# Optimization experiments

Hardware: AMD Instinct MI355X
Metric: run time of the kernel (lower is better)

The kernel has to match this reference:

```python
import jax, jax.numpy as jnp
import numpy as np
from jax import lax

IN, H1, H2, F1, OUT = 26, 64, 32, 16, 10
B, T = 512, 1000


def _lstm(x, w_ih, w_hh, b_ih, b_hh):
    """PyTorch-convention LSTM (gate order i,f,g,o). x: [B,T,I].
    Returns (all hidden states [B,T,H], final hidden [B,H])."""
    Bx = x.shape[0]
    H = w_hh.shape[1]
    # Precompute input projections for all timesteps: [B,T,4H]
    xg = jnp.einsum('bti,gi->btg', x, w_ih) + b_ih + b_hh

    def step(carry, xg_t):
        h, c = carry
        gates = xg_t + h @ w_hh.T  # [B,4H]
        i, f, g, o = jnp.split(gates, 4, axis=-1)
        i = jax.nn.sigmoid(i)
        f = jax.nn.sigmoid(f)
        g = jnp.tanh(g)
        o = jax.nn.sigmoid(o)
        c = f * c + i * g
        h = o * jnp.tanh(c)
        return (h, c), h

    init = (jnp.zeros((Bx, H), x.dtype), jnp.zeros((Bx, H), x.dtype))
    (h_last, _), hs = lax.scan(step, init, xg.transpose(1, 0, 2))
    return hs.transpose(1, 0, 2), h_last


def setup_inputs() -> dict:
    key = jax.random.key(0)
    ks = jax.random.split(key, 14)

    def u(k, shape, fan):
        bound = 1.0 / np.sqrt(fan)
        return jax.random.uniform(k, shape, jnp.float32, -bound, bound)

    return {
        'x': jax.random.normal(ks[0], (B, 1, IN, T), jnp.float32),
        'w_ih1': u(ks[1], (4 * H1, IN), H1),
        'w_hh1': u(ks[2], (4 * H1, H1), H1),
        'b_ih1': u(ks[3], (4 * H1,), H1),
        'b_hh1': u(ks[4], (4 * H1,), H1),
        'w_ih2': u(ks[5], (4 * H2, H1), H2),
        'w_hh2': u(ks[6], (4 * H2, H2), H2),
        'b_ih2': u(ks[7], (4 * H2,), H2),
        'b_hh2': u(ks[8], (4 * H2,), H2),
        'w_fc1': u(ks[9], (F1, H2), H2),
        'b_fc1': u(ks[10], (F1,), H2),
        'w_fc2': u(ks[11], (OUT, F1), F1),
        'b_fc2': u(ks[12], (OUT,), F1),
    }


def reference(x, w_ih1, w_hh1, b_ih1, b_hh1, w_ih2, w_hh2, b_ih2, b_hh2,
              w_fc1, b_fc1, w_fc2, b_fc2):
    # [B,1,26,T] -> [B,26,T] -> [B,T,26]
    x = jnp.transpose(x[:, 0], (0, 2, 1))
    out1, _ = _lstm(x, w_ih1, w_hh1, b_ih1, b_hh1)
    # Dropout is identity in eval mode.
    _, h2 = _lstm(out1, w_ih2, w_hh2, b_ih2, b_hh2)  # final hidden [B,32]
    h = jax.nn.relu(h2 @ w_fc1.T + b_fc1)
    return h @ w_fc2.T + b_fc2  # [B,10]
```

## Files before the change

kernel.cpp:

```cpp
#include <hip/hip_runtime.h>
#include <hip/hip_bf16.h>


typedef __hip_bfloat16 bf16;
typedef _Float16 f16;
typedef _Float16 f16x8 __attribute__((ext_vector_type(8)));
typedef _Float16 f16x4 __attribute__((ext_vector_type(4)));
typedef float    f32x4 __attribute__((ext_vector_type(4)));

#define T_STEPS 1000
#define IN_DIM  26
#define EPB     16
#define CH      16
#define NCHUNK  62
#define H1P     72
#define H2P     40
#define XP      40

#define NL2E  -1.4426950408889634f
#define N2L2E -2.8853900817779268f

__device__ __forceinline__ float bits2f(unsigned short h) {
    return __uint_as_float(((unsigned int)h) << 16);
}
__device__ __forceinline__ float ldv(const void* p, long i, bool isb) {
    return isb ? bits2f(((const unsigned short*)p)[i]) : ((const float*)p)[i];
}
__device__ __forceinline__ float rcp_(float x) { return __builtin_amdgcn_rcpf(x); }
__device__ __forceinline__ float ex2_(float x) { return __builtin_amdgcn_exp2f(x); }

__device__ __forceinline__ float lstm_act(float yi, float yf, float yg,
                                          float yo, float& c) {
    const float A  = ex2_(yi), F = ex2_(yf), B = ex2_(yg), O = ex2_(yo);
    const float a1 = 1.f + A, f1 = 1.f + F, b1 = 1.f + B, o1 = 1.f + O;
    const float ig = (2.f - b1) * rcp_(a1 * b1);
    c = fmaf(rcp_(f1), c, ig);
    const float C2  = ex2_(N2L2E * c);
    const float c1p = 1.f + C2;
    return (2.f - c1p) * rcp_(o1 * c1p);
}

#define MFMA(a, b, c) __builtin_amdgcn_mfma_f32_16x16x32_f16((a), (b), (c), 0, 0, 0)

__global__
__attribute__((amdgpu_flat_work_group_size(512, 512), amdgpu_waves_per_eu(2, 2)))
void lstm_fused(const void* __restrict__ x,
                const void* __restrict__ w_ih1, const void* __restrict__ w_hh1,
                const void* __restrict__ b_ih1, const void* __restrict__ b_hh1,
                const void* __restrict__ w_ih2, const void* __restrict__ w_hh2,
                const void* __restrict__ b_ih2, const void* __restrict__ b_hh2,
                const void* __restrict__ w_fc1, const void* __restrict__ b_fc1,
                const void* __restrict__ w_fc2, const void* __restrict__ b_fc2,
                void* __restrict__ out)
{
    const int tid  = threadIdx.x;
    const int lane = tid & 63;
    const int wv   = tid >> 6;
    const int ecol = lane & 15;
    const int g4   = lane >> 4;
    const int r15  = lane & 15;
    const int e0   = blockIdx.x * EPB;

    __shared__ __align__(16) f16   Xst[2][CH][EPB][XP];
    __shared__ __align__(16) f16   H1T[2][EPB][H1P];
    __shared__ __align__(16) f16   H2T[2][EPB][H2P];
    __shared__ __align__(16) float f1s[EPB][16];

    bool isb = true;
    {
        const unsigned short* wu = (const unsigned short*)w_ih1;
        for (int k = 0; k < 64; ++k) {
            float v = fabsf(bits2f(wu[k]));
            if (!(v <= 0.1251f)) isb = false;
        }
    }

    {
        float4 z; z.x = z.y = z.z = z.w = 0.f;
        float4* p = (float4*)&Xst[0][0][0][0];
        for (int k = tid; k < (int)(sizeof(Xst) / 16); k += 512) p[k] = z;
        float4* q = (float4*)&H1T[0][0][0];
        for (int k = tid; k < (int)(sizeof(H1T) / 16); k += 512) q[k] = z;
        float4* r = (float4*)&H2T[0][0][0];
        for (int k = tid; k < (int)(sizeof(H2T) / 16); k += 512) r[k] = z;
    }

    f16x8 W8[8]; f16x8 W4[4]; f32x4 C4[4];
    if (wv < 4) {
#pragma unroll
        for (int gi = 0; gi < 4; ++gi) {
            const float sc = (gi == 2) ? N2L2E : NL2E;
            const int R = gi * 64 + 16 * wv + r15;
#pragma unroll
            for (int k0 = 0; k0 < 2; ++k0)
#pragma unroll
                for (int jj = 0; jj < 8; ++jj)
                    W8[gi * 2 + k0][jj] =
                        (f16)(sc * ldv(w_hh1, R * 64 + k0 * 32 + g4 * 8 + jj, isb));
#pragma unroll
            for (int jj = 0; jj < 8; ++jj) {
                const int k = g4 * 8 + jj;
                W4[gi][jj] =
                    (f16)(k < IN_DIM ? sc * ldv(w_ih1, R * IN_DIM + k, isb) : 0.f);
            }
#pragma unroll
            for (int jj = 0; jj < 4; ++jj) {
                const int Rc = gi * 64 + 16 * wv + g4 * 4 + jj;
                C4[gi][jj] = sc * (ldv(b_ih1, Rc, isb) + ldv(b_hh1, Rc, isb));
            }
        }
    } else if (wv < 6) {
        const int hf = wv - 4;
#pragma unroll
        for (int gi = 0; gi < 4; ++gi) {
            const float sc = (gi == 2) ? N2L2E : NL2E;
            const int R = gi * 32 + 16 * hf + r15;
#pragma unroll
            for (int k0 = 0; k0 < 2; ++k0)
#pragma unroll
                for (int jj = 0; jj < 8; ++jj)
                    W8[gi * 2 + k0][jj] =
                        (f16)(sc * ldv(w_ih2, R * 64 + k0 * 32 + g4 * 8 + jj, isb));
#pragma unroll
            for (int jj = 0; jj < 8; ++jj)
                W4[gi][jj] = (f16)(sc * ldv(w_hh2, R * 32 + g4 * 8 + jj, isb));
#pragma unroll
            for (int jj = 0; jj < 4; ++jj) {
                const int Rc = gi * 32 + 16 * hf + g4 * 4 + jj;
                C4[gi][jj] = sc * (ldv(b_ih2, Rc, isb) + ldv(b_hh2, Rc, isb));
            }
        }
    }

    __syncthreads();

    auto stageRow = [&](int p, int c) {
        const int t0 = c * CH;
        const int nt = (T_STEPS - t0 < CH) ? (T_STEPS - t0) : CH;
        const int e = p / IN_DIM, i = p - e * IN_DIM;
        const long gb = ((long)(e0 + e) * IN_DIM + i) * T_STEPS + t0;
        float4 fb[4];
        if (isb) {
            const float4* q = (const float4*)((const unsigned short*)x + gb);
            fb[0] = q[0]; if (nt > 8) fb[1] = q[1];
        } else {
            const float4* q = (const float4*)((const float*)x + gb);
            fb[0] = q[0]; fb[1] = q[1];
            if (nt > 8) { fb[2] = q[2]; fb[3] = q[3]; }
        }
#pragma unroll
        for (int t = 0; t < CH; ++t) if (t < nt) {
            float v;
            if (isb) {
                unsigned int u =
                    __builtin_bit_cast(unsigned int, fb[t >> 3][(t >> 1) & 3]);
                v = bits2f((t & 1) ? (unsigned short)(u >> 16)
                                   : (unsigned short)(u & 0xffffu));
            } else {
                v = fb[t >> 2][t & 3];
            }
            Xst[c & 1][t][e][i] = (f16)v;
        }
    };

    if (tid < EPB * IN_DIM) stageRow(tid, 0);
    if (tid >= 448 && tid < 448 + 26) stageRow(tid - 448, 1);
    __syncthreads();

    f32x4 xgc[4];
    if (wv < 4) {
        const f16x8 xf = *(const f16x8*)&Xst[0][0][ecol][g4 * 8];
#pragma unroll
        for (int gi = 0; gi < 4; ++gi) xgc[gi] = MFMA(W4[gi], xf, C4[gi]);
    }

    if (wv < 6) __builtin_amdgcn_s_setprio(1);

    float cst[4] = {0.f, 0.f, 0.f, 0.f};

    for (int s = 0; s <= T_STEPS; ++s) {
        const int pc = s & 1, pp = pc ^ 1;

        if (wv < 4) {
            if (s < T_STEPS) {
                const f16x8 h1f0 = *(const f16x8*)&H1T[pp][ecol][g4 * 8];
                const f16x8 h1f1 = *(const f16x8*)&H1T[pp][ecol][32 + g4 * 8];
                const bool nx = (s + 1 < T_STEPS);
                f16x8 xf = {};
                if (nx) {
                    const int sn = s + 1;
                    xf = *(const f16x8*)&Xst[(sn >> 4) & 1][sn & 15][ecol][g4 * 8];
                }
                f32x4 gt[4];
#pragma unroll
                for (int gi = 0; gi < 4; ++gi) {
                    f32x4 t0 = MFMA(W8[gi * 2 + 0], h1f0, xgc[gi]);
                    gt[gi]   = MFMA(W8[gi * 2 + 1], h1f1, t0);
                }
                f32x4 xgn[4];
                if (nx) {
#pragma unroll
                    for (int gi = 0; gi < 4; ++gi)
                        xgn[gi] = MFMA(W4[gi], xf, C4[gi]);
                }
                f16x4 hh;
#pragma unroll
                for (int jj = 0; jj < 4; ++jj)
                    hh[jj] = (f16)lstm_act(gt[0][jj], gt[1][jj],
                                           gt[2][jj], gt[3][jj], cst[jj]);
                *(f16x4*)&H1T[pc][ecol][16 * wv + g4 * 4] = hh;
                if (nx) {
#pragma unroll
                    for (int gi = 0; gi < 4; ++gi) xgc[gi] = xgn[gi];
                }
            }
        } else if (wv < 6) {
            if (s >= 1) {
                const int hf = wv - 4;
                const f16x8 h1f0 = *(const f16x8*)&H1T[pp][ecol][g4 * 8];
                const f16x8 h1f1 = *(const f16x8*)&H1T[pp][ecol][32 + g4 * 8];
                const f16x8 h2f  = *(const f16x8*)&H2T[pc][ecol][g4 * 8];
                f32x4 gt[4];
#pragma unroll
                for (int gi = 0; gi < 4; ++gi) {
                    f32x4 t0 = MFMA(W8[gi * 2 + 0], h1f0, C4[gi]);
                    t0       = MFMA(W8[gi * 2 + 1], h1f1, t0);
                    gt[gi]   = MFMA(W4[gi], h2f, t0);
                }
                f16x4 hh;
#pragma unroll
                for (int jj = 0; jj < 4; ++jj)
                    hh[jj] = (f16)lstm_act(gt[0][jj], gt[1][jj],
                                           gt[2][jj], gt[3][jj], cst[jj]);
                *(f16x4*)&H2T[pp][ecol][16 * hf + g4 * 4] = hh;
            }
        } else {
            const int s1 = s + 1, c = (s1 >> 4) + 1;
            if (c <= NCHUNK) {
                const int slice = s1 & 15;
                const int p = slice * 26 + (wv - 6) * 13 + lane;
                if (lane < 13) stageRow(p, c);
            }
        }

        __syncthreads();
    }

    if (tid < EPB * 16) {
        const int e = tid >> 4, o = tid & 15;
        float ss = ldv(b_fc1, o, isb);
#pragma unroll 8
        for (int k = 0; k < 32; ++k)
            ss = fmaf(ldv(w_fc1, o * 32 + k, isb), (float)H2T[1][e][k], ss);
        f1s[e][o] = fmaxf(ss, 0.f);
    }
    __syncthreads();
    if (tid < EPB * 10) {
        const int e = tid / 10, o = tid - e * 10;
        float ss = ldv(b_fc2, o, isb);
#pragma unroll
        for (int k = 0; k < 16; ++k)
            ss = fmaf(ldv(w_fc2, o * 16 + k, isb), f1s[e][k], ss);
        const long oi = (long)(e0 + e) * 10 + o;
        if (isb) ((bf16*)out)[oi] = __float2bfloat16(ss);
        else     ((float*)out)[oi] = ss;
    }
}

extern "C" void kernel_launch(void* const* d_in, const int* in_sizes, int n_in,
                              void* d_out, int out_size, void* d_ws, size_t ws_size,
                              hipStream_t stream) {
    lstm_fused<<<dim3(512 / EPB), dim3(512), 0, stream>>>(
        d_in[0], d_in[1], d_in[2], d_in[3], d_in[4],
        d_in[5], d_in[6], d_in[7], d_in[8],
        d_in[9], d_in[10], d_in[11], d_in[12], d_out);
}
```

Before: 821.7 us.

## Process two 16-sequence groups per block with interleaved layer-1 MFMA chains

Each block now handles 32 sequences as two groups: the four layer-1 waves compute both groups' recurrences interleaved, and waves 4-7 split layer-2 work across the groups instead of waves 6-7 doing input staging. Global staging loads are spread across all waves, issued at loop start and written to LDS after compute to hide latency. The grid halves to 16 blocks, so fewer CUs are used, but the independent X/Y chains give more instruction-level parallelism inside the latency-bound recurrent step. The cost is doubled per-step work for layer-1 waves and higher register pressure.

```diff
diff --git a/kernel.cpp b/kernel.cpp
--- a/kernel.cpp
+++ b/kernel.cpp
@@ -59,12 +59,12 @@
     const int ecol = lane & 15;
     const int g4   = lane >> 4;
     const int r15  = lane & 15;
-    const int e0   = blockIdx.x * EPB;
-
-    __shared__ __align__(16) f16   Xst[2][CH][EPB][XP];
-    __shared__ __align__(16) f16   H1T[2][EPB][H1P];
-    __shared__ __align__(16) f16   H2T[2][EPB][H2P];
-    __shared__ __align__(16) float f1s[EPB][16];
+    const int e00  = blockIdx.x * (2 * EPB);
+
+    __shared__ __align__(16) f16   Xst[2][2][CH][EPB][XP];
+    __shared__ __align__(16) f16   H1T[2][2][EPB][H1P];
+    __shared__ __align__(16) f16   H2T[2][2][EPB][H2P];
+    __shared__ __align__(16) float f1s[2][EPB][16];
 
     bool isb = true;
     {
@@ -77,11 +77,11 @@
 
     {
         float4 z; z.x = z.y = z.z = z.w = 0.f;
-        float4* p = (float4*)&Xst[0][0][0][0];
+        float4* p = (float4*)&Xst[0][0][0][0][0];
         for (int k = tid; k < (int)(sizeof(Xst) / 16); k += 512) p[k] = z;
-        float4* q = (float4*)&H1T[0][0][0];
+        float4* q = (float4*)&H1T[0][0][0][0];
         for (int k = tid; k < (int)(sizeof(H1T) / 16); k += 512) q[k] = z;
-        float4* r = (float4*)&H2T[0][0][0];
+        float4* r = (float4*)&H2T[0][0][0][0];
         for (int k = tid; k < (int)(sizeof(H2T) / 16); k += 512) r[k] = z;
     }
 
@@ -109,8 +109,8 @@
                 C4[gi][jj] = sc * (ldv(b_ih1, Rc, isb) + ldv(b_hh1, Rc, isb));
             }
         }
-    } else if (wv < 6) {
-        const int hf = wv - 4;
+    } else {
+        const int hf = (wv - 4) & 1;
 #pragma unroll
         for (int gi = 0; gi < 4; ++gi) {
             const float sc = (gi == 2) ? N2L2E : NL2E;
@@ -134,11 +134,11 @@
 
     __syncthreads();
 
-    auto stageRow = [&](int p, int c) {
+    auto stageP = [&](int g, int p, int c) {
         const int t0 = c * CH;
         const int nt = (T_STEPS - t0 < CH) ? (T_STEPS - t0) : CH;
         const int e = p / IN_DIM, i = p - e * IN_DIM;
-        const long gb = ((long)(e0 + e) * IN_DIM + i) * T_STEPS + t0;
+        const long gb = ((long)(e00 + g * EPB + e) * IN_DIM + i) * T_STEPS + t0;
         float4 fb[4];
         if (isb) {
             const float4* q = (const float4*)((const unsigned short*)x + gb);
@@ -159,67 +159,107 @@
             } else {
                 v = fb[t >> 2][t & 3];
             }
-            Xst[c & 1][t][e][i] = (f16)v;
+            Xst[g][c & 1][t][e][i] = (f16)v;
         }
     };
 
-    if (tid < EPB * IN_DIM) stageRow(tid, 0);
-    if (tid >= 448 && tid < 448 + 26) stageRow(tid - 448, 1);
+    for (int r = tid; r < 2 * EPB * IN_DIM; r += 512)
+        stageP(r / (EPB * IN_DIM), r % (EPB * IN_DIM), 0);
+    if (tid >= 460) {
+        const int r = tid - 460;
+        stageP(r / IN_DIM, r % IN_DIM, 1);
+    }
     __syncthreads();
 
-    f32x4 xgc[4];
+    f32x4 xgcX[4], xgcY[4];
     if (wv < 4) {
-        const f16x8 xf = *(const f16x8*)&Xst[0][0][ecol][g4 * 8];
-#pragma unroll
-        for (int gi = 0; gi < 4; ++gi) xgc[gi] = MFMA(W4[gi], xf, C4[gi]);
-    }
-
-    if (wv < 6) __builtin_amdgcn_s_setprio(1);
-
+        const f16x8 xfX = *(const f16x8*)&Xst[0][0][0][ecol][g4 * 8];
+        const f16x8 xfY = *(const f16x8*)&Xst[1][0][0][ecol][g4 * 8];
+#pragma unroll
+        for (int gi = 0; gi < 4; ++gi) {
+            xgcX[gi] = MFMA(W4[gi], xfX, C4[gi]);
+            xgcY[gi] = MFMA(W4[gi], xfY, C4[gi]);
+        }
+    }
+
+    float c1X[4] = {0.f, 0.f, 0.f, 0.f};
+    float c1Y[4] = {0.f, 0.f, 0.f, 0.f};
     float cst[4] = {0.f, 0.f, 0.f, 0.f};
+
+    const int srow = wv + 8 * lane;
+    const bool stl = (srow < 52);
+    const int sG = stl ? (srow / IN_DIM) : 0;
+    const int sI = stl ? (srow - sG * IN_DIM) : 0;
 
     for (int s = 0; s <= T_STEPS; ++s) {
         const int pc = s & 1, pp = pc ^ 1;
 
+        const int s1 = s + 1, cS = (s1 >> 4) + 1;
+        const bool doS = stl && (cS <= NCHUNK);
+        float4 fbS[4];
+        int eS = 0, ntS = CH;
+        if (doS) {
+            eS = s1 & 15;
+            const int t0S = cS * CH;
+            ntS = (T_STEPS - t0S < CH) ? (T_STEPS - t0S) : CH;
+            const long gb =
+                ((long)(e00 + sG * EPB + eS) * IN_DIM + sI) * T_STEPS + t0S;
+            if (isb) {
+                const float4* q = (const float4*)((const unsigned short*)x + gb);
+                fbS[0] = q[0]; if (ntS > 8) fbS[1] = q[1];
+            } else {
+                const float4* q = (const float4*)((const float*)x + gb);
+                fbS[0] = q[0]; fbS[1] = q[1];
+                if (ntS > 8) { fbS[2] = q[2]; fbS[3] = q[3]; }
+            }
+        }
+
         if (wv < 4) {
             if (s < T_STEPS) {
-                const f16x8 h1f0 = *(const f16x8*)&H1T[pp][ecol][g4 * 8];
-                const f16x8 h1f1 = *(const f16x8*)&H1T[pp][ecol][32 + g4 * 8];
+                const f16x8 h1f0X = *(const f16x8*)&H1T[0][pp][ecol][g4 * 8];
+                const f16x8 h1f1X = *(const f16x8*)&H1T[0][pp][ecol][32 + g4 * 8];
+                const f16x8 h1f0Y = *(const f16x8*)&H1T[1][pp][ecol][g4 * 8];
+                const f16x8 h1f1Y = *(const f16x8*)&H1T[1][pp][ecol][32 + g4 * 8];
                 const bool nx = (s + 1 < T_STEPS);
-                f16x8 xf = {};
+                f16x8 xfX = {}, xfY = {};
                 if (nx) {
-                    const int sn = s + 1;
-                    xf = *(const f16x8*)&Xst[(sn >> 4) & 1][sn & 15][ecol][g4 * 8];
-                }
-                f32x4 gt[4];
+                    const int sn = s + 1, nb = (sn >> 4) & 1, nt = sn & 15;
+                    xfX = *(const f16x8*)&Xst[0][nb][nt][ecol][g4 * 8];
+                    xfY = *(const f16x8*)&Xst[1][nb][nt][ecol][g4 * 8];
+                }
+                f32x4 gtX[4], gtY[4];
 #pragma unroll
                 for (int gi = 0; gi < 4; ++gi) {
-                    f32x4 t0 = MFMA(W8[gi * 2 + 0], h1f0, xgc[gi]);
-                    gt[gi]   = MFMA(W8[gi * 2 + 1], h1f1, t0);
-                }
-                f32x4 xgn[4];
+                    f32x4 tX = MFMA(W8[gi * 2 + 0], h1f0X, xgcX[gi]);
+                    gtX[gi]  = MFMA(W8[gi * 2 + 1], h1f1X, tX);
+                    f32x4 tY = MFMA(W8[gi * 2 + 0], h1f0Y, xgcY[gi]);
+                    gtY[gi]  = MFMA(W8[gi * 2 + 1], h1f1Y, tY);
+                }
                 if (nx) {
 #pragma unroll
-                    for (int gi = 0; gi < 4; ++gi)
-                        xgn[gi] = MFMA(W4[gi], xf, C4[gi]);
-                }
-                f16x4 hh;
-#pragma unroll
-                for (int jj = 0; jj < 4; ++jj)
-                    hh[jj] = (f16)lstm_act(gt[0][jj], gt[1][jj],
-                                           gt[2][jj], gt[3][jj], cst[jj]);
-                *(f16x4*)&H1T[pc][ecol][16 * wv + g4 * 4] = hh;
-                if (nx) {
-#pragma unroll
-                    for (int gi = 0; gi < 4; ++gi) xgc[gi] = xgn[gi];
-                }
-            }
-        } else if (wv < 6) {
+                    for (int gi = 0; gi < 4; ++gi) {
+                        xgcX[gi] = MFMA(W4[gi], xfX, C4[gi]);
+                        xgcY[gi] = MFMA(W4[gi], xfY, C4[gi]);
+                    }
+                }
+                f16x4 hhX, hhY;
+#pragma unroll
+                for (int jj = 0; jj < 4; ++jj) {
+                    hhX[jj] = (f16)lstm_act(gtX[0][jj], gtX[1][jj],
+                                            gtX[2][jj], gtX[3][jj], c1X[jj]);
+                    hhY[jj] = (f16)lstm_act(gtY[0][jj], gtY[1][jj],
+                                            gtY[2][jj], gtY[3][jj], c1Y[jj]);
+                }
+                *(f16x4*)&H1T[0][pc][ecol][16 * wv + g4 * 4] = hhX;
+                *(f16x4*)&H1T[1][pc][ecol][16 * wv + g4 * 4] = hhY;
+            }
+        } else {
             if (s >= 1) {
-                const int hf = wv - 4;
-                const f16x8 h1f0 = *(const f16x8*)&H1T[pp][ecol][g4 * 8];
-                const f16x8 h1f1 = *(const f16x8*)&H1T[pp][ecol][32 + g4 * 8];
-                const f16x8 h2f  = *(const f16x8*)&H2T[pc][ecol][g4 * 8];
+                const int g  = (wv >= 6) ? 1 : 0;
+                const int hf = (wv - 4) & 1;
+                const f16x8 h1f0 = *(const f16x8*)&H1T[g][pp][ecol][g4 * 8];
+                const f16x8 h1f1 = *(const f16x8*)&H1T[g][pp][ecol][32 + g4 * 8];
+                const f16x8 h2f  = *(const f16x8*)&H2T[g][pc][ecol][g4 * 8];
                 f32x4 gt[4];
 #pragma unroll
                 for (int gi = 0; gi < 4; ++gi) {
@@ -232,36 +272,48 @@
                 for (int jj = 0; jj < 4; ++jj)
                     hh[jj] = (f16)lstm_act(gt[0][jj], gt[1][jj],
                                            gt[2][jj], gt[3][jj], cst[jj]);
-                *(f16x4*)&H2T[pp][ecol][16 * hf + g4 * 4] = hh;
-            }
-        } else {
-            const int s1 = s + 1, c = (s1 >> 4) + 1;
-            if (c <= NCHUNK) {
-                const int slice = s1 & 15;
-                const int p = slice * 26 + (wv - 6) * 13 + lane;
-                if (lane < 13) stageRow(p, c);
+                *(f16x4*)&H2T[g][pp][ecol][16 * hf + g4 * 4] = hh;
+            }
+        }
+
+        if (doS) {
+            const int bf = cS & 1;
+#pragma unroll
+            for (int t = 0; t < CH; ++t) if (t < ntS) {
+                float v;
+                if (isb) {
+                    unsigned int u =
+                        __builtin_bit_cast(unsigned int, fbS[t >> 3][(t >> 1) & 3]);
+                    v = bits2f((t & 1) ? (unsigned short)(u >> 16)
+                                       : (unsigned short)(u & 0xffffu));
+                } else {
+                    v = fbS[t >> 2][t & 3];
+                }
+                Xst[sG][bf][t][eS][sI] = (f16)v;
             }
         }
 
         __syncthreads();
     }
 
-    if (tid < EPB * 16) {
-        const int e = tid >> 4, o = tid & 15;
+    {
+        const int g = tid >> 8, r = tid & 255;
+        const int e = r >> 4, o = r & 15;
         float ss = ldv(b_fc1, o, isb);
 #pragma unroll 8
         for (int k = 0; k < 32; ++k)
-            ss = fmaf(ldv(w_fc1, o * 32 + k, isb), (float)H2T[1][e][k], ss);
-        f1s[e][o] = fmaxf(ss, 0.f);
+            ss = fmaf(ldv(w_fc1, o * 32 + k, isb), (float)H2T[g][1][e][k], ss);
+        f1s[g][e][o] = fmaxf(ss, 0.f);
     }
     __syncthreads();
-    if (tid < EPB * 10) {
-        const int e = tid / 10, o = tid - e * 10;
+    if (tid < 320) {
+        const int g = tid / 160, r = tid - g * 160;
+        const int e = r / 10, o = r - e * 10;
         float ss = ldv(b_fc2, o, isb);
 #pragma unroll
         for (int k = 0; k < 16; ++k)
-            ss = fmaf(ldv(w_fc2, o * 16 + k, isb), f1s[e][k], ss);
-        const long oi = (long)(e0 + e) * 10 + o;
+            ss = fmaf(ldv(w_fc2, o * 16 + k, isb), f1s[g][e][k], ss);
+        const long oi = (long)(e00 + g * EPB + e) * 10 + o;
         if (isb) ((bf16*)out)[oi] = __float2bfloat16(ss);
         else     ((float*)out)[oi] = ss;
     }
@@ -270,7 +322,7 @@
 extern "C" void kernel_launch(void* const* d_in, const int* in_sizes, int n_in,
                               void* d_out, int out_size, void* d_ws, size_t ws_size,
                               hipStream_t stream) {
-    lstm_fused<<<dim3(512 / EPB), dim3(512), 0, stream>>>(
+    lstm_fused<<<dim3(512 / (2 * EPB)), dim3(512), 0, stream>>>(
         d_in[0], d_in[1], d_in[2], d_in[3], d_in[4],
         d_in[5], d_in[6], d_in[7], d_in[8],
         d_in[9], d_in[10], d_in[11], d_in[12], d_out);
```

Result: slower. 2.414 ms (+193.8%).

## Merge LSTM layer roles into four uniform waves, bulk-stage input every chunk

Applied to the files above, without the earlier changes.

Replaces the specialised wave roles (4 layer-1 waves, 2 layer-2 waves, 2 loader waves) with 4 waves that each compute a layer-1 slice and a duplicated layer-2 slice. Each wave applies the activation to half of the layer-2 outputs. Input staging becomes a bulk load of a whole 16-step chunk once every 16 steps. The cell update is rewritten to use one reciprocal instead of two. The aim is fewer waves per barrier and less cost on the serial per-step critical path. The trade-off is redundant layer-2 MFMAs, more registers per wave, and periodic load stalls at chunk boundaries that no longer overlap with compute.

```diff
diff --git a/kernel.cpp b/kernel.cpp
--- a/kernel.cpp
+++ b/kernel.cpp
@@ -6,13 +6,13 @@
 typedef _Float16 f16;
 typedef _Float16 f16x8 __attribute__((ext_vector_type(8)));
 typedef _Float16 f16x4 __attribute__((ext_vector_type(4)));
+typedef _Float16 f16x2 __attribute__((ext_vector_type(2)));
 typedef float    f32x4 __attribute__((ext_vector_type(4)));
 
 #define T_STEPS 1000
 #define IN_DIM  26
 #define EPB     16
 #define CH      16
-#define NCHUNK  62
 #define H1P     72
 #define H2P     40
 #define XP      40
@@ -33,8 +33,9 @@
                                           float yo, float& c) {
     const float A  = ex2_(yi), F = ex2_(yf), B = ex2_(yg), O = ex2_(yo);
     const float a1 = 1.f + A, f1 = 1.f + F, b1 = 1.f + B, o1 = 1.f + O;
-    const float ig = (2.f - b1) * rcp_(a1 * b1);
-    c = fmaf(rcp_(f1), c, ig);
+    const float P  = a1 * b1;
+    const float R  = rcp_(P * f1);
+    c = R * fmaf(c, P, (2.f - b1) * f1);
     const float C2  = ex2_(N2L2E * c);
     const float c1p = 1.f + C2;
     return (2.f - c1p) * rcp_(o1 * c1p);
@@ -43,7 +44,7 @@
 #define MFMA(a, b, c) __builtin_amdgcn_mfma_f32_16x16x32_f16((a), (b), (c), 0, 0, 0)
 
 __global__
-__attribute__((amdgpu_flat_work_group_size(512, 512), amdgpu_waves_per_eu(2, 2)))
+__attribute__((amdgpu_flat_work_group_size(256, 256), amdgpu_waves_per_eu(1, 1)))
 void lstm_fused(const void* __restrict__ x,
                 const void* __restrict__ w_ih1, const void* __restrict__ w_hh1,
                 const void* __restrict__ b_ih1, const void* __restrict__ b_hh1,
@@ -56,6 +57,8 @@
     const int tid  = threadIdx.x;
     const int lane = tid & 63;
     const int wv   = tid >> 6;
+    const int hf   = wv & 1;
+    const int jh   = wv >> 1;
     const int ecol = lane & 15;
     const int g4   = lane >> 4;
     const int r15  = lane & 15;
@@ -78,56 +81,53 @@
     {
         float4 z; z.x = z.y = z.z = z.w = 0.f;
         float4* p = (float4*)&Xst[0][0][0][0];
-        for (int k = tid; k < (int)(sizeof(Xst) / 16); k += 512) p[k] = z;
+        for (int k = tid; k < (int)(sizeof(Xst) / 16); k += 256) p[k] = z;
         float4* q = (float4*)&H1T[0][0][0];
-        for (int k = tid; k < (int)(sizeof(H1T) / 16); k += 512) q[k] = z;
+        for (int k = tid; k < (int)(sizeof(H1T) / 16); k += 256) q[k] = z;
         float4* r = (float4*)&H2T[0][0][0];
-        for (int k = tid; k < (int)(sizeof(H2T) / 16); k += 512) r[k] = z;
-    }
-
-    f16x8 W8[8]; f16x8 W4[4]; f32x4 C4[4];
-    if (wv < 4) {
-#pragma unroll
-        for (int gi = 0; gi < 4; ++gi) {
-            const float sc = (gi == 2) ? N2L2E : NL2E;
+        for (int k = tid; k < (int)(sizeof(H2T) / 16); k += 256) r[k] = z;
+    }
+
+    f16x8 Whh1A[8]; f16x8 Wih1A[4]; f32x4 b1C[4];
+    f16x8 Wih2A[8]; f16x8 Whh2A[4]; f32x4 b2C[4];
+#pragma unroll
+    for (int gi = 0; gi < 4; ++gi) {
+        const float sc = (gi == 2) ? N2L2E : NL2E;
+        {
             const int R = gi * 64 + 16 * wv + r15;
 #pragma unroll
             for (int k0 = 0; k0 < 2; ++k0)
 #pragma unroll
                 for (int jj = 0; jj < 8; ++jj)
-                    W8[gi * 2 + k0][jj] =
+                    Whh1A[gi * 2 + k0][jj] =
                         (f16)(sc * ldv(w_hh1, R * 64 + k0 * 32 + g4 * 8 + jj, isb));
 #pragma unroll
             for (int jj = 0; jj < 8; ++jj) {
                 const int k = g4 * 8 + jj;
-                W4[gi][jj] =
+                Wih1A[gi][jj] =
                     (f16)(k < IN_DIM ? sc * ldv(w_ih1, R * IN_DIM + k, isb) : 0.f);
             }
 #pragma unroll
             for (int jj = 0; jj < 4; ++jj) {
                 const int Rc = gi * 64 + 16 * wv + g4 * 4 + jj;
-                C4[gi][jj] = sc * (ldv(b_ih1, Rc, isb) + ldv(b_hh1, Rc, isb));
-            }
-        }
-    } else if (wv < 6) {
-        const int hf = wv - 4;
-#pragma unroll
-        for (int gi = 0; gi < 4; ++gi) {
-            const float sc = (gi == 2) ? N2L2E : NL2E;
+                b1C[gi][jj] = sc * (ldv(b_ih1, Rc, isb) + ldv(b_hh1, Rc, isb));
+            }
+        }
+        {
             const int R = gi * 32 + 16 * hf + r15;
 #pragma unroll
             for (int k0 = 0; k0 < 2; ++k0)
 #pragma unroll
                 for (int jj = 0; jj < 8; ++jj)
-                    W8[gi * 2 + k0][jj] =
+                    Wih2A[gi * 2 + k0][jj] =
                         (f16)(sc * ldv(w_ih2, R * 64 + k0 * 32 + g4 * 8 + jj, isb));
 #pragma unroll
             for (int jj = 0; jj < 8; ++jj)
-                W4[gi][jj] = (f16)(sc * ldv(w_hh2, R * 32 + g4 * 8 + jj, isb));
+                Whh2A[gi][jj] = (f16)(sc * ldv(w_hh2, R * 32 + g4 * 8 + jj, isb));
 #pragma unroll
             for (int jj = 0; jj < 4; ++jj) {
                 const int Rc = gi * 32 + 16 * hf + g4 * 4 + jj;
-                C4[gi][jj] = sc * (ldv(b_ih2, Rc, isb) + ldv(b_hh2, Rc, isb));
+                b2C[gi][jj] = sc * (ldv(b_ih2, Rc, isb) + ldv(b_hh2, Rc, isb));
             }
         }
     }
@@ -163,90 +163,86 @@
         }
     };
 
-    if (tid < EPB * IN_DIM) stageRow(tid, 0);
-    if (tid >= 448 && tid < 448 + 26) stageRow(tid - 448, 1);
+    for (int p = tid; p < EPB * IN_DIM; p += 256) stageRow(p, 0);
     __syncthreads();
 
     f32x4 xgc[4];
-    if (wv < 4) {
+    {
         const f16x8 xf = *(const f16x8*)&Xst[0][0][ecol][g4 * 8];
 #pragma unroll
-        for (int gi = 0; gi < 4; ++gi) xgc[gi] = MFMA(W4[gi], xf, C4[gi]);
-    }
-
-    if (wv < 6) __builtin_amdgcn_s_setprio(1);
-
-    float cst[4] = {0.f, 0.f, 0.f, 0.f};
+        for (int gi = 0; gi < 4; ++gi) xgc[gi] = MFMA(Wih1A[gi], xf, b1C[gi]);
+    }
+
+    float c1s[4] = {0.f, 0.f, 0.f, 0.f};
+    float c2s[2] = {0.f, 0.f};
 
     for (int s = 0; s <= T_STEPS; ++s) {
         const int pc = s & 1, pp = pc ^ 1;
 
-        if (wv < 4) {
-            if (s < T_STEPS) {
-                const f16x8 h1f0 = *(const f16x8*)&H1T[pp][ecol][g4 * 8];
-                const f16x8 h1f1 = *(const f16x8*)&H1T[pp][ecol][32 + g4 * 8];
-                const bool nx = (s + 1 < T_STEPS);
-                f16x8 xf = {};
-                if (nx) {
-                    const int sn = s + 1;
-                    xf = *(const f16x8*)&Xst[(sn >> 4) & 1][sn & 15][ecol][g4 * 8];
-                }
-                f32x4 gt[4];
-#pragma unroll
-                for (int gi = 0; gi < 4; ++gi) {
-                    f32x4 t0 = MFMA(W8[gi * 2 + 0], h1f0, xgc[gi]);
-                    gt[gi]   = MFMA(W8[gi * 2 + 1], h1f1, t0);
-                }
-                f32x4 xgn[4];
-                if (nx) {
-#pragma unroll
-                    for (int gi = 0; gi < 4; ++gi)
-                        xgn[gi] = MFMA(W4[gi], xf, C4[gi]);
-                }
-                f16x4 hh;
-#pragma unroll
-                for (int jj = 0; jj < 4; ++jj)
-                    hh[jj] = (f16)lstm_act(gt[0][jj], gt[1][jj],
-                                           gt[2][jj], gt[3][jj], cst[jj]);
-                *(f16x4*)&H1T[pc][ecol][16 * wv + g4 * 4] = hh;
-                if (nx) {
-#pragma unroll
-                    for (int gi = 0; gi < 4; ++gi) xgc[gi] = xgn[gi];
-                }
-            }
-        } else if (wv < 6) {
-            if (s >= 1) {
-                const int hf = wv - 4;
-                const f16x8 h1f0 = *(const f16x8*)&H1T[pp][ecol][g4 * 8];
-                const f16x8 h1f1 = *(const f16x8*)&H1T[pp][ecol][32 + g4 * 8];
-                const f16x8 h2f  = *(const f16x8*)&H2T[pc][ecol][g4 * 8];
-                f32x4 gt[4];
-#pragma unroll
-                for (int gi = 0; gi < 4; ++gi) {
-                    f32x4 t0 = MFMA(W8[gi * 2 + 0], h1f0, C4[gi]);
-                    t0       = MFMA(W8[gi * 2 + 1], h1f1, t0);
-                    gt[gi]   = MFMA(W4[gi], h2f, t0);
-                }
-                f16x4 hh;
-#pragma unroll
-                for (int jj = 0; jj < 4; ++jj)
-                    hh[jj] = (f16)lstm_act(gt[0][jj], gt[1][jj],
-                                           gt[2][jj], gt[3][jj], cst[jj]);
-                *(f16x4*)&H2T[pp][ecol][16 * hf + g4 * 4] = hh;
-            }
-        } else {
-            const int s1 = s + 1, c = (s1 >> 4) + 1;
-            if (c <= NCHUNK) {
-                const int slice = s1 & 15;
-                const int p = slice * 26 + (wv - 6) * 13 + lane;
-                if (lane < 13) stageRow(p, c);
-            }
+        const f16x8 h1f0 = *(const f16x8*)&H1T[pp][ecol][g4 * 8];
+        const f16x8 h1f1 = *(const f16x8*)&H1T[pp][ecol][32 + g4 * 8];
+        const f16x8 h2f  = *(const f16x8*)&H2T[pc][ecol][g4 * 8];
+        const bool nx = (s + 1 < T_STEPS);
+        f16x8 xf = {};
+        if (nx) {
+            const int sn = s + 1;
+            xf = *(const f16x8*)&Xst[(sn >> 4) & 1][sn & 15][ecol][g4 * 8];
+        }
+
+        f32x4 gt1[4], xgn[4], gt2[4];
+        if (s < T_STEPS) {
+#pragma unroll
+            for (int gi = 0; gi < 4; ++gi) {
+                f32x4 t0 = MFMA(Whh1A[gi * 2 + 0], h1f0, xgc[gi]);
+                gt1[gi]  = MFMA(Whh1A[gi * 2 + 1], h1f1, t0);
+            }
+            if (nx) {
+#pragma unroll
+                for (int gi = 0; gi < 4; ++gi)
+                    xgn[gi] = MFMA(Wih1A[gi], xf, b1C[gi]);
+            }
+        }
+        if (s >= 1) {
+#pragma unroll
+            for (int gi = 0; gi < 4; ++gi) {
+                f32x4 t0 = MFMA(Wih2A[gi * 2 + 0], h1f0, b2C[gi]);
+                t0       = MFMA(Wih2A[gi * 2 + 1], h1f1, t0);
+                gt2[gi]  = MFMA(Whh2A[gi], h2f, t0);
+            }
+        }
+
+        if (s < T_STEPS) {
+            f16x4 hh;
+#pragma unroll
+            for (int jj = 0; jj < 4; ++jj)
+                hh[jj] = (f16)lstm_act(gt1[0][jj], gt1[1][jj],
+                                       gt1[2][jj], gt1[3][jj], c1s[jj]);
+            *(f16x4*)&H1T[pc][ecol][16 * wv + g4 * 4] = hh;
+            if (nx) {
+#pragma unroll
+                for (int gi = 0; gi < 4; ++gi) xgc[gi] = xgn[gi];
+            }
+        }
+        if (s >= 1) {
+            f16x2 hh;
+#pragma unroll
+            for (int q = 0; q < 2; ++q) {
+                const int jj = 2 * jh + q;
+                hh[q] = (f16)lstm_act(gt2[0][jj], gt2[1][jj],
+                                      gt2[2][jj], gt2[3][jj], c2s[q]);
+            }
+            *(f16x2*)&H2T[pp][ecol][16 * hf + g4 * 4 + 2 * jh] = hh;
+        }
+
+        if ((s & (CH - 1)) == 0 && s + CH < T_STEPS) {
+            const int c = (s >> 4) + 1;
+            for (int p = tid; p < EPB * IN_DIM; p += 256) stageRow(p, c);
         }
 
         __syncthreads();
     }
 
-    if (tid < EPB * 16) {
+    {
         const int e = tid >> 4, o = tid & 15;
         float ss = ldv(b_fc1, o, isb);
 #pragma unroll 8
@@ -270,7 +266,7 @@
 extern "C" void kernel_launch(void* const* d_in, const int* in_sizes, int n_in,
                               void* d_out, int out_size, void* d_ws, size_t ws_size,
                               hipStream_t stream) {
-    lstm_fused<<<dim3(512 / EPB), dim3(512), 0, stream>>>(
+    lstm_fused<<<dim3(512 / EPB), dim3(256), 0, stream>>>(
         d_in[0], d_in[1], d_in[2], d_in[3], d_in[4],
         d_in[5], d_in[6], d_in[7], d_in[8],
         d_in[9], d_in[10], d_in[11], d_in[12], d_out);
```

Measured after the change: 1.121 ms. 36.5% more time.
